# Optimization experiments

Hardware: AMD Instinct MI355X
Metric: run time of the kernel (lower is better)

## Reference

```python
import jax, jax.numpy as jnp
import numpy as np

PAD = 1
STRIDE = 1


def setup_inputs() -> dict:
    key = jax.random.key(0)
    k1, k2 = jax.random.split(key)
    B, C, H, W = 16, 64, 112, 112
    KS, O = 3, 128
    x = jax.random.normal(k1, (B, C, H, W), dtype=jnp.float32)
    # weight layout matches torch module: (in_channel, k, k, out_channel)
    weight = jax.random.normal(k2, (C, KS, KS, O), dtype=jnp.float32)
    return {"x": x, "weight": weight}


def reference(x, weight):
    # Original: pad -> im2col (B,Ho,Wo,C*k*k) -> matmul with weight.reshape(-1,O)
    # -> permute to (B,O,Ho,Wo). This is exactly a standard conv2d; we express
    # it as the fused implicit-GEMM convolution (same math, no huge intermediate).
    # Note: the module's _bias parameter is never used in forward, so no bias here.
    w_oihw = jnp.transpose(weight, (3, 0, 1, 2))  # (O, C, kh, kw)
    out = jax.lax.conv_general_dilated(
        x,
        w_oihw,
        window_strides=(STRIDE, STRIDE),
        padding=[(PAD, PAD), (PAD, PAD)],
        dimension_numbers=("NCHW", "OIHW", "NCHW"),
    )
    return out  # (B, O, Ho, Wo)
```

## Files before the change

### kernel.cpp

```cpp
#include <hip/hip_runtime.h>
#include <hip/hip_bf16.h>
#include <stdint.h>

typedef __attribute__((ext_vector_type(8))) short short8;
typedef __attribute__((ext_vector_type(4))) float f32x4;

#define B_   16
#define C_   64
#define H_   112
#define W_   112
#define O_   128
#define HP   114
#define HWP  (HP*HP)
#define HW   (H_*W_)
#define XPAD_BYTES ((size_t)B_*HWP*C_*2)
#define NROWS 384

__device__ __forceinline__ unsigned short f2bf(float f) {
    union { float f; uint32_t u; } v; v.f = f;
    uint32_t u = v.u;
    u += 0x7fffu + ((u >> 16) & 1u);
    return (unsigned short)(u >> 16);
}

__global__ void prep(const float* __restrict__ x, const float* __restrict__ wt,
                     unsigned short* __restrict__ xpad,
                     unsigned short* __restrict__ wbuf)
{
    const int t = threadIdx.x;
    if (blockIdx.x >= B_ * H_) {
        int f = (blockIdx.x - B_ * H_) * 256 + t;
        int j    = f & 7;
        int lane = (f >> 3) & 63;
        int nf   = (f >> 9) & 3;
        int wc   = (f >> 11) & 1;
        int ks   = (f >> 12) & 1;
        int s    = f >> 13;
        int o = wc * 64 + nf * 16 + (lane & 15);
        int c = (ks * 4 + (lane >> 4)) * 8 + j;
        int kh = s / 3, kw = s % 3;
        wbuf[f] = f2bf(wt[(((size_t)c * 3 + kh) * 3 + kw) * O_ + o]);
        return;
    }

    __shared__ float tile[64][114];
    const int bh = blockIdx.x;
    const int b = bh / H_, h = bh % H_;

    const float* xr = x + ((size_t)b * C_ * HW) + (size_t)h * W_;
    #pragma unroll
    for (int i = 0; i < 7; ++i) {
        int flat = i * 256 + t;
        int c = flat / 28, w4 = flat % 28;
        f32x4 v = __builtin_nontemporal_load(
            (const f32x4*)(xr + (size_t)c * HW + (size_t)w4 * 4));
        *(float2*)&tile[c][w4 * 4]     = make_float2(v.x, v.y);
        *(float2*)&tile[c][w4 * 4 + 2] = make_float2(v.z, v.w);
    }

    if (t < 64) {
        size_t base = ((size_t)(b * HP + h + 1) * HP) * 64;
        xpad[base + t] = 0;
        xpad[base + (size_t)113 * 64 + t] = 0;
    }
    if (h == 0 || h == 111) {
        const int row = (h == 0) ? 0 : 113;
        size_t base = ((size_t)(b * HP + row) * HP) * 64;
        ushort4 z4; z4.x = z4.y = z4.z = z4.w = 0;
        for (int k = t; k < (HP * 64) / 4; k += 256)
            *(ushort4*)(xpad + base + (size_t)k * 4) = z4;
    }
    __syncthreads();

    unsigned short* dst = xpad + ((size_t)(b * HP + h + 1) * HP + 1) * C_;
    #pragma unroll
    for (int j = 0; j < 7; ++j) {
        int flat = j * 256 + t;
        int w = flat >> 4, c = (flat & 15) * 4;
        ushort4 v;
        v.x = f2bf(tile[c + 0][w]);
        v.y = f2bf(tile[c + 1][w]);
        v.z = f2bf(tile[c + 2][w]);
        v.w = f2bf(tile[c + 3][w]);
        *(ushort4*)(dst + (size_t)w * C_ + c) = v;
    }
}

__global__ __launch_bounds__(256, 3) void conv_gemm(
    const char* __restrict__ xpad,
    const char* __restrict__ wbuf,
    float* __restrict__ out)
{
    __shared__ char ldsA[NROWS * 128];

    const int t = threadIdx.x;
    const int lane = t & 63, wid = t >> 6;
    const int wr = wid >> 1, wc = wid & 1;
    const int bid0 = blockIdx.x;
    const int bid = (bid0 & 7) * 196 + (bid0 >> 3);
    const int b = bid / 98;
    const int ml0 = (bid % 98) * 128;
    const int oh0 = ml0 / W_;
    const int pbase = ml0 + 2 * oh0;

    const char* plane = xpad + (size_t)b * ((size_t)HWP * 128);
    #pragma unroll
    for (int i = 0; i < 12; ++i) {
        const int gbase = i * 256 + wid * 64;
        const int g = gbase + lane;
        const int r = g >> 3, ck = g & 7;
        __builtin_amdgcn_global_load_lds(
            (const __attribute__((address_space(1))) void*)
                (plane + (size_t)(pbase + r) * 128 + ((ck ^ (r & 7)) << 4)),
            (__attribute__((address_space(3))) void*)(ldsA + gbase * 16),
            16, 0, 0);
    }
    __syncthreads();

    int rowb[4];
    #pragma unroll
    for (int mf = 0; mf < 4; ++mf) {
        int ml = ml0 + wr * 64 + mf * 16 + (lane & 15);
        int oh = ml / W_;
        rowb[mf] = ml + 2 * oh - pbase;
    }
    const int kq = lane >> 4;

    f32x4 acc[4][4] = {};

    #pragma unroll
    for (int s = 0; s < 9; ++s) {
        const int kh = s / 3, kw = s % 3;
        const int soff = kh * HP + kw;
        const char* wb = (const char*)wbuf + s * 16384 + wc * 4096 + lane * 16;

        #pragma unroll
        for (int ks = 0; ks < 2; ++ks) {
            short8 bv[4];
            #pragma unroll
            for (int nf = 0; nf < 4; ++nf)
                bv[nf] = *(const short8*)(wb + ks * 8192 + nf * 1024);

            short8 av[4];
            #pragma unroll
            for (int mf = 0; mf < 4; ++mf) {
                const int lrow = rowb[mf] + soff;
                const int ck = (ks * 4 + kq) ^ (lrow & 7);
                av[mf] = *(const short8*)(ldsA + lrow * 128 + (ck << 4));
            }
            __builtin_amdgcn_s_setprio(1);
            #pragma unroll
            for (int mf = 0; mf < 4; ++mf)
                #pragma unroll
                for (int nf = 0; nf < 4; ++nf)
                    acc[mf][nf] = __builtin_amdgcn_mfma_f32_16x16x32_bf16(
                        av[mf], bv[nf], acc[mf][nf], 0, 0, 0);
            __builtin_amdgcn_s_setprio(0);
        }
    }

    const int oc = wc * 64 + (lane & 15);
    const int mrow = ml0 + wr * 64 + ((lane >> 4) << 2);
    #pragma unroll
    for (int mf = 0; mf < 4; ++mf) {
        #pragma unroll
        for (int nf = 0; nf < 4; ++nf) {
            float* dst = out + ((size_t)(b * O_ + oc + nf * 16) * HW) + mrow + mf * 16;
            __builtin_nontemporal_store(acc[mf][nf], (f32x4*)dst);
        }
    }
}

extern "C" void kernel_launch(void* const* d_in, const int* in_sizes, int n_in,
                              void* d_out, int out_size, void* d_ws, size_t ws_size,
                              hipStream_t stream) {
    const float* x  = (const float*)d_in[0];
    const float* wt = (const float*)d_in[1];
    float* out = (float*)d_out;
    char* xpad = (char*)d_ws;
    char* wbuf = (char*)d_ws + XPAD_BYTES;

    hipLaunchKernelGGL(prep, dim3(B_ * H_ + 288), dim3(256), 0, stream,
                       x, wt, (unsigned short*)xpad, (unsigned short*)wbuf);
    hipLaunchKernelGGL(conv_gemm, dim3(1568), dim3(256), 0, stream,
                       xpad, wbuf, out);
}
```

Before: 70.09 us.

## Stage weight slices through double-buffered LDS instead of direct global reads

Each 3x3 tap's 16KB weight slice is now loaded into a double-buffered LDS region with global_load_lds. The next tap is prefetched while the current one is computed, with a block barrier after each tap. The activation tile shrinks to 368 rows to make room, occupancy drops from 3 to 2 blocks per CU, and output stores become regular stores instead of nontemporal. This removes repeated global/L2 weight reads per wave, at the cost of lower occupancy and per-tap synchronisation.

```diff
diff --git a/kernel.cpp b/kernel.cpp
--- a/kernel.cpp
+++ b/kernel.cpp
@@ -14,7 +14,7 @@
 #define HWP  (HP*HP)
 #define HW   (H_*W_)
 #define XPAD_BYTES ((size_t)B_*HWP*C_*2)
-#define NROWS 384
+#define NROWS 368
 
 __device__ __forceinline__ unsigned short f2bf(float f) {
     union { float f; uint32_t u; } v; v.f = f;
@@ -86,12 +86,14 @@
     }
 }
 
-__global__ __launch_bounds__(256, 3) void conv_gemm(
+__global__ __launch_bounds__(256, 2) void conv_gemm(
     const char* __restrict__ xpad,
     const char* __restrict__ wbuf,
     float* __restrict__ out)
 {
-    __shared__ char ldsA[NROWS * 128];
+    __shared__ char lds[NROWS * 128 + 2 * 16384];
+    char* ldsA = lds;
+    char* ldsB = lds + NROWS * 128;
 
     const int t = threadIdx.x;
     const int lane = t & 63, wid = t >> 6;
@@ -106,13 +108,24 @@
     const char* plane = xpad + (size_t)b * ((size_t)HWP * 128);
     #pragma unroll
     for (int i = 0; i < 12; ++i) {
-        const int gbase = i * 256 + wid * 64;
-        const int g = gbase + lane;
-        const int r = g >> 3, ck = g & 7;
+        if (i < 11 || wid < 2) {
+            const int gbase = i * 256 + wid * 64;
+            const int g = gbase + lane;
+            const int r = g >> 3, ck = g & 7;
+            __builtin_amdgcn_global_load_lds(
+                (const __attribute__((address_space(1))) void*)
+                    (plane + (size_t)(pbase + r) * 128 + ((ck ^ (r & 7)) << 4)),
+                (__attribute__((address_space(3))) void*)(ldsA + gbase * 16),
+                16, 0, 0);
+        }
+    }
+    #pragma unroll
+    for (int i = 0; i < 4; ++i) {
+        const int gb = i * 256 + wid * 64;
         __builtin_amdgcn_global_load_lds(
             (const __attribute__((address_space(1))) void*)
-                (plane + (size_t)(pbase + r) * 128 + ((ck ^ (r & 7)) << 4)),
-            (__attribute__((address_space(3))) void*)(ldsA + gbase * 16),
+                ((const char*)wbuf + (size_t)(gb + lane) * 16),
+            (__attribute__((address_space(3))) void*)(ldsB + gb * 16),
             16, 0, 0);
     }
     __syncthreads();
@@ -130,16 +143,29 @@
 
     #pragma unroll
     for (int s = 0; s < 9; ++s) {
-        const int kh = s / 3, kw = s % 3;
-        const int soff = kh * HP + kw;
-        const char* wb = (const char*)wbuf + s * 16384 + wc * 4096 + lane * 16;
+        if (s < 8) {
+            const char* wsl = (const char*)wbuf + (s + 1) * 16384;
+            char* dstB = ldsB + ((s + 1) & 1) * 16384;
+            #pragma unroll
+            for (int i = 0; i < 4; ++i) {
+                const int gb = i * 256 + wid * 64;
+                __builtin_amdgcn_global_load_lds(
+                    (const __attribute__((address_space(1))) void*)
+                        (wsl + (size_t)(gb + lane) * 16),
+                    (__attribute__((address_space(3))) void*)(dstB + gb * 16),
+                    16, 0, 0);
+            }
+        }
+
+        const int soff = (s / 3) * HP + (s % 3);
+        const char* bbase = ldsB + (s & 1) * 16384 + wc * 4096 + lane * 16;
 
         #pragma unroll
         for (int ks = 0; ks < 2; ++ks) {
             short8 bv[4];
             #pragma unroll
             for (int nf = 0; nf < 4; ++nf)
-                bv[nf] = *(const short8*)(wb + ks * 8192 + nf * 1024);
+                bv[nf] = *(const short8*)(bbase + ks * 8192 + nf * 1024);
 
             short8 av[4];
             #pragma unroll
@@ -157,6 +183,7 @@
                         av[mf], bv[nf], acc[mf][nf], 0, 0, 0);
             __builtin_amdgcn_s_setprio(0);
         }
+        if (s < 8) __syncthreads();
     }
 
     const int oc = wc * 64 + (lane & 15);
@@ -166,7 +193,7 @@
         #pragma unroll
         for (int nf = 0; nf < 4; ++nf) {
             float* dst = out + ((size_t)(b * O_ + oc + nf * 16) * HW) + mrow + mf * 16;
-            __builtin_nontemporal_store(acc[mf][nf], (f32x4*)dst);
+            *(f32x4*)dst = acc[mf][nf];
         }
     }
 }
```

Result: faster. 64.91 us (-7.4%).

## Make conv GEMM persistent with double-buffered LDS prefetch of input tiles

Applied to the files above, without the earlier changes.

Replaces the 1568-block one-tile-per-block launch with 256 persistent 512-thread blocks. Each block walks 6-7 tiles in an XCD-aware order and prefetches the next tile's padded input rows into a second LDS buffer while computing the current one. Waves now cover 32 rows each, with fewer accumulators. Output stores become plain instead of nontemporal. The aim is to hide global-to-LDS load latency and cut launch and tail overhead, at the cost of less occupancy flexibility and uneven per-block tile counts.

```diff
diff --git a/kernel.cpp b/kernel.cpp
--- a/kernel.cpp
+++ b/kernel.cpp
@@ -14,7 +14,7 @@
 #define HWP  (HP*HP)
 #define HW   (H_*W_)
 #define XPAD_BYTES ((size_t)B_*HWP*C_*2)
-#define NROWS 384
+#define NROWS 368
 
 __device__ __forceinline__ unsigned short f2bf(float f) {
     union { float f; uint32_t u; } v; v.f = f;
@@ -86,87 +86,101 @@
     }
 }
 
-__global__ __launch_bounds__(256, 3) void conv_gemm(
+__global__ __launch_bounds__(512, 2) void conv_gemm(
     const char* __restrict__ xpad,
     const char* __restrict__ wbuf,
     float* __restrict__ out)
 {
-    __shared__ char ldsA[NROWS * 128];
+    __shared__ char lds[2][NROWS * 128];
 
     const int t = threadIdx.x;
     const int lane = t & 63, wid = t >> 6;
     const int wr = wid >> 1, wc = wid & 1;
-    const int bid0 = blockIdx.x;
-    const int bid = (bid0 & 7) * 196 + (bid0 >> 3);
-    const int b = bid / 98;
-    const int ml0 = (bid % 98) * 128;
-    const int oh0 = ml0 / W_;
-    const int pbase = ml0 + 2 * oh0;
-
-    const char* plane = xpad + (size_t)b * ((size_t)HWP * 128);
-    #pragma unroll
-    for (int i = 0; i < 12; ++i) {
-        const int gbase = i * 256 + wid * 64;
-        const int g = gbase + lane;
-        const int r = g >> 3, ck = g & 7;
-        __builtin_amdgcn_global_load_lds(
-            (const __attribute__((address_space(1))) void*)
-                (plane + (size_t)(pbase + r) * 128 + ((ck ^ (r & 7)) << 4)),
-            (__attribute__((address_space(3))) void*)(ldsA + gbase * 16),
-            16, 0, 0);
-    }
-    __syncthreads();
-
-    int rowb[4];
-    #pragma unroll
-    for (int mf = 0; mf < 4; ++mf) {
-        int ml = ml0 + wr * 64 + mf * 16 + (lane & 15);
-        int oh = ml / W_;
-        rowb[mf] = ml + 2 * oh - pbase;
-    }
+    const int p = blockIdx.x;
+    const int xcd = p & 7, slot = p >> 3;
+    const int ntiles = (slot < 4) ? 7 : 6;
     const int kq = lane >> 4;
 
-    f32x4 acc[4][4] = {};
-
-    #pragma unroll
-    for (int s = 0; s < 9; ++s) {
-        const int kh = s / 3, kw = s % 3;
-        const int soff = kh * HP + kw;
-        const char* wb = (const char*)wbuf + s * 16384 + wc * 4096 + lane * 16;
-
-        #pragma unroll
-        for (int ks = 0; ks < 2; ++ks) {
-            short8 bv[4];
+    auto stage = [&](char* buf, int g) {
+        const int ml0r = (g % 98) * 128;
+        const int pb = ml0r + 2 * (ml0r / W_);
+        const char* plane = xpad + (size_t)(g / 98) * ((size_t)HWP * 128);
+        #pragma unroll
+        for (int i = 0; i < 6; ++i) {
+            if (i < 5 || wid < 6) {
+                const int gb = i * 512 + wid * 64;
+                const int u = gb + lane;
+                const int r = u >> 3, ck = u & 7;
+                __builtin_amdgcn_global_load_lds(
+                    (const __attribute__((address_space(1))) void*)
+                        (plane + (size_t)(pb + r) * 128 + ((ck ^ (r & 7)) << 4)),
+                    (__attribute__((address_space(3))) void*)(buf + gb * 16),
+                    16, 0, 0);
+            }
+        }
+    };
+
+    int g = xcd * 196 + slot;
+    stage(lds[0], g);
+
+    for (int j = 0; j < ntiles; ++j, g += 32) {
+        const int b = g / 98;
+        const int ml0 = (g % 98) * 128;
+        const int pbase = ml0 + 2 * (ml0 / W_);
+
+        __syncthreads();
+        if (j + 1 < ntiles) stage(lds[(j + 1) & 1], g + 32);
+        const char* A = lds[j & 1];
+
+        int rowb[2];
+        #pragma unroll
+        for (int mf = 0; mf < 2; ++mf) {
+            int ml = ml0 + wr * 32 + mf * 16 + (lane & 15);
+            rowb[mf] = ml + 2 * (ml / W_) - pbase;
+        }
+
+        f32x4 acc[2][4] = {};
+
+        #pragma unroll
+        for (int s = 0; s < 9; ++s) {
+            const int soff = (s / 3) * HP + (s % 3);
+            const char* wb = wbuf + s * 16384 + wc * 4096 + lane * 16;
+
             #pragma unroll
-            for (int nf = 0; nf < 4; ++nf)
-                bv[nf] = *(const short8*)(wb + ks * 8192 + nf * 1024);
-
-            short8 av[4];
-            #pragma unroll
-            for (int mf = 0; mf < 4; ++mf) {
-                const int lrow = rowb[mf] + soff;
-                const int ck = (ks * 4 + kq) ^ (lrow & 7);
-                av[mf] = *(const short8*)(ldsA + lrow * 128 + (ck << 4));
-            }
-            __builtin_amdgcn_s_setprio(1);
-            #pragma unroll
-            for (int mf = 0; mf < 4; ++mf)
+            for (int ks = 0; ks < 2; ++ks) {
+                short8 bv[4];
                 #pragma unroll
                 for (int nf = 0; nf < 4; ++nf)
-                    acc[mf][nf] = __builtin_amdgcn_mfma_f32_16x16x32_bf16(
-                        av[mf], bv[nf], acc[mf][nf], 0, 0, 0);
-            __builtin_amdgcn_s_setprio(0);
-        }
-    }
-
-    const int oc = wc * 64 + (lane & 15);
-    const int mrow = ml0 + wr * 64 + ((lane >> 4) << 2);
-    #pragma unroll
-    for (int mf = 0; mf < 4; ++mf) {
-        #pragma unroll
-        for (int nf = 0; nf < 4; ++nf) {
-            float* dst = out + ((size_t)(b * O_ + oc + nf * 16) * HW) + mrow + mf * 16;
-            __builtin_nontemporal_store(acc[mf][nf], (f32x4*)dst);
+                    bv[nf] = *(const short8*)(wb + ks * 8192 + nf * 1024);
+
+                short8 av[2];
+                #pragma unroll
+                for (int mf = 0; mf < 2; ++mf) {
+                    const int lrow = rowb[mf] + soff;
+                    const int ck = (ks * 4 + kq) ^ (lrow & 7);
+                    av[mf] = *(const short8*)(A + lrow * 128 + (ck << 4));
+                }
+                __builtin_amdgcn_s_setprio(1);
+                #pragma unroll
+                for (int mf = 0; mf < 2; ++mf)
+                    #pragma unroll
+                    for (int nf = 0; nf < 4; ++nf)
+                        acc[mf][nf] = __builtin_amdgcn_mfma_f32_16x16x32_bf16(
+                            av[mf], bv[nf], acc[mf][nf], 0, 0, 0);
+                __builtin_amdgcn_s_setprio(0);
+            }
+        }
+
+        const int oc = wc * 64 + (lane & 15);
+        const int mrow = ml0 + wr * 32 + ((lane >> 4) << 2);
+        #pragma unroll
+        for (int mf = 0; mf < 2; ++mf) {
+            #pragma unroll
+            for (int nf = 0; nf < 4; ++nf) {
+                float* dst = out + ((size_t)(b * O_ + oc + nf * 16) * HW)
+                           + mrow + mf * 16;
+                *(f32x4*)dst = acc[mf][nf];
+            }
         }
     }
 }
@@ -182,6 +196,6 @@
 
     hipLaunchKernelGGL(prep, dim3(B_ * H_ + 288), dim3(256), 0, stream,
                        x, wt, (unsigned short*)xpad, (unsigned short*)wbuf);
-    hipLaunchKernelGGL(conv_gemm, dim3(1568), dim3(256), 0, stream,
+    hipLaunchKernelGGL(conv_gemm, dim3(256), dim3(512), 0, stream,
                        xpad, wbuf, out);
 }
```

Result: slower. 136.3 us (+94.5%).

## Read conv input tiles directly from global memory instead of LDS staging

Applied to the files above, without the earlier changes.

Removes the LDS staging of the padded input halo (global_load_lds plus barrier) and has each wave load its A fragments straight from global memory through the cache. It also raises the occupancy hint to 4 blocks per CU, stops unrolling the 9-tap loop, and replaces the nontemporal output stores with plain stores. This drops the LDS footprint and the block-wide sync, at the cost of redundant global/L2 traffic for overlapping taps and higher load latency inside the MFMA loop.

```diff
diff --git a/kernel.cpp b/kernel.cpp
--- a/kernel.cpp
+++ b/kernel.cpp
@@ -14,7 +14,6 @@
 #define HWP  (HP*HP)
 #define HW   (H_*W_)
 #define XPAD_BYTES ((size_t)B_*HWP*C_*2)
-#define NROWS 384
 
 __device__ __forceinline__ unsigned short f2bf(float f) {
     union { float f; uint32_t u; } v; v.f = f;
@@ -86,13 +85,11 @@
     }
 }
 
-__global__ __launch_bounds__(256, 3) void conv_gemm(
+__global__ __launch_bounds__(256, 4) void conv_gemm(
     const char* __restrict__ xpad,
     const char* __restrict__ wbuf,
     float* __restrict__ out)
 {
-    __shared__ char ldsA[NROWS * 128];
-
     const int t = threadIdx.x;
     const int lane = t & 63, wid = t >> 6;
     const int wr = wid >> 1, wc = wid & 1;
@@ -100,54 +97,36 @@
     const int bid = (bid0 & 7) * 196 + (bid0 >> 3);
     const int b = bid / 98;
     const int ml0 = (bid % 98) * 128;
-    const int oh0 = ml0 / W_;
-    const int pbase = ml0 + 2 * oh0;
+    const int kq = lane >> 4;
 
     const char* plane = xpad + (size_t)b * ((size_t)HWP * 128);
-    #pragma unroll
-    for (int i = 0; i < 12; ++i) {
-        const int gbase = i * 256 + wid * 64;
-        const int g = gbase + lane;
-        const int r = g >> 3, ck = g & 7;
-        __builtin_amdgcn_global_load_lds(
-            (const __attribute__((address_space(1))) void*)
-                (plane + (size_t)(pbase + r) * 128 + ((ck ^ (r & 7)) << 4)),
-            (__attribute__((address_space(3))) void*)(ldsA + gbase * 16),
-            16, 0, 0);
-    }
-    __syncthreads();
 
-    int rowb[4];
+    const char* abase[4];
     #pragma unroll
     for (int mf = 0; mf < 4; ++mf) {
         int ml = ml0 + wr * 64 + mf * 16 + (lane & 15);
         int oh = ml / W_;
-        rowb[mf] = ml + 2 * oh - pbase;
+        abase[mf] = plane + (size_t)(ml + 2 * oh) * 128 + (kq << 4);
     }
-    const int kq = lane >> 4;
+    const char* wb0 = wbuf + wc * 4096 + lane * 16;
 
     f32x4 acc[4][4] = {};
 
-    #pragma unroll
+    #pragma unroll 1
     for (int s = 0; s < 9; ++s) {
-        const int kh = s / 3, kw = s % 3;
-        const int soff = kh * HP + kw;
-        const char* wb = (const char*)wbuf + s * 16384 + wc * 4096 + lane * 16;
+        const int aoff = ((s / 3) * HP + (s % 3)) * 128;
+        const char* wb = wb0 + s * 16384;
 
         #pragma unroll
         for (int ks = 0; ks < 2; ++ks) {
-            short8 bv[4];
+            short8 bv[4], av[4];
             #pragma unroll
             for (int nf = 0; nf < 4; ++nf)
                 bv[nf] = *(const short8*)(wb + ks * 8192 + nf * 1024);
+            #pragma unroll
+            for (int mf = 0; mf < 4; ++mf)
+                av[mf] = *(const short8*)(abase[mf] + aoff + ks * 64);
 
-            short8 av[4];
-            #pragma unroll
-            for (int mf = 0; mf < 4; ++mf) {
-                const int lrow = rowb[mf] + soff;
-                const int ck = (ks * 4 + kq) ^ (lrow & 7);
-                av[mf] = *(const short8*)(ldsA + lrow * 128 + (ck << 4));
-            }
             __builtin_amdgcn_s_setprio(1);
             #pragma unroll
             for (int mf = 0; mf < 4; ++mf)
@@ -166,7 +145,7 @@
         #pragma unroll
         for (int nf = 0; nf < 4; ++nf) {
             float* dst = out + ((size_t)(b * O_ + oc + nf * 16) * HW) + mrow + mf * 16;
-            __builtin_nontemporal_store(acc[mf][nf], (f32x4*)dst);
+            *(f32x4*)dst = acc[mf][nf];
         }
     }
 }
```

After: 105.6 us. 50.6% more time.
